# Performance work log

Measured on AMD Instinct MI355X. Metric: run time of the kernel, lower is better.

The kernel has to match this reference:

```python
import jax, jax.numpy as jnp
import numpy as np

N = 100000
E = 1600000
F_IN, H, C = 128, 128, 64


def setup_inputs() -> dict:
    key = jax.random.key(0)
    ks = jax.random.split(key, 8)
    x = jax.random.normal(ks[0], (N, F_IN), dtype=jnp.float32)
    edge_index = jax.random.randint(ks[1], (2, E), 0, N, dtype=jnp.int64)
    s = lambda fi: (1.0 / np.sqrt(fi))
    # SAGEConv1: lin_l (applied to mean-aggregated neighbors, has bias), lin_r (root, no bias)
    W1l = jax.random.uniform(ks[2], (H, F_IN), jnp.float32, -s(F_IN), s(F_IN))
    b1 = jnp.zeros((H,), jnp.float32)
    W1r = jax.random.uniform(ks[3], (H, F_IN), jnp.float32, -s(F_IN), s(F_IN))
    # SAGEConv2
    W2l = jax.random.uniform(ks[4], (C, H), jnp.float32, -s(H), s(H))
    b2 = jnp.zeros((C,), jnp.float32)
    W2r = jax.random.uniform(ks[5], (C, H), jnp.float32, -s(H), s(H))
    return {"x": x, "edge_index": edge_index, "W1l": W1l, "b1": b1, "W1r": W1r,
            "W2l": W2l, "b2": b2, "W2r": W2r}


def _mean_aggr(x, src, dst):
    # mean over incoming neighbors (PyG flow: edge_index[0]=source -> edge_index[1]=target)
    msg = x[src]                                            # [E, F] big gather
    summed = jax.ops.segment_sum(msg, dst, num_segments=N)  # [N, F]
    cnt = jax.ops.segment_sum(jnp.ones((src.shape[0],), x.dtype), dst, num_segments=N)
    return summed / jnp.clip(cnt, 1.0)[:, None]


def _sage_conv(x, src, dst, Wl, b, Wr):
    agg = _mean_aggr(x, src, dst)
    return agg @ Wl.T + b + x @ Wr.T


def _iconv(x, src, dst):
    # weight-free GCN propagation: D^-1/2 (A + I) D^-1/2 @ x
    loops = jnp.arange(N, dtype=src.dtype)
    s2 = jnp.concatenate([src, loops])
    d2 = jnp.concatenate([dst, loops])
    deg = jax.ops.segment_sum(jnp.ones((s2.shape[0],), x.dtype), d2, num_segments=N)
    dis = jnp.where(deg > 0, jax.lax.rsqrt(jnp.maximum(deg, 1.0)), 0.0)
    norm = dis[s2] * dis[d2]                               # [E+N]
    return jax.ops.segment_sum(norm[:, None] * x[s2], d2, num_segments=N)


def reference(x, edge_index, W1l, b1, W1r, W2l, b2, W2r):
    src, dst = edge_index[0], edge_index[1]
    h = jax.nn.relu(_sage_conv(x, src, dst, W1l, b1, W1r))
    # F.dropout(training=False) -> identity in eval mode
    h = _sage_conv(h, src, dst, W2l, b2, W2r)
    return _iconv(h, src, dst)
```

## Files before the change

### kernel.cpp

```cpp
#include <hip/hip_runtime.h>

#define GN 100000
#define GE 1600000
#define GF 128
#define GH 128
#define GC 64

#define NB 392
#define SLABSZ 5376
#define P1_EDGES 4096
#define P1_BLOCKS ((GE + P1_EDGES - 1) / P1_EDGES)
#define CASTX_BLOCKS 12500

typedef __attribute__((ext_vector_type(8))) short v8s;
typedef __attribute__((ext_vector_type(4))) float v4f;

__device__ __forceinline__ unsigned short f2bf(float f) {
    union { float f; unsigned u; } a; a.f = f;
    unsigned r = a.u + 0x7fff + ((a.u >> 16) & 1);
    return (unsigned short)(r >> 16);
}
__device__ __forceinline__ float bf2f(unsigned short b) {
    union { unsigned u; float f; } a; a.u = ((unsigned)b) << 16;
    return a.f;
}

__global__ __launch_bounds__(256) void prep_kernel(
    unsigned* __restrict__ slab, int* __restrict__ bucket_cnt,
    const int* __restrict__ src, const int* __restrict__ dst,
    unsigned short* __restrict__ xb, const float* __restrict__ x,
    unsigned short* w1l, unsigned short* w1r,
    unsigned short* w2l, unsigned short* w2r,
    const float* W1l, const float* W1r,
    const float* W2l, const float* W2r)
{
    __shared__ int hist[512];
    __shared__ int scanex[512];
    __shared__ int cursor[512];
    __shared__ int gbase[512];
    __shared__ int ssum[256];
    __shared__ unsigned stage[P1_EDGES];
    __shared__ unsigned short sbid[P1_EDGES];

    int tid = threadIdx.x;
    int blk = blockIdx.x;

    if (blk >= P1_BLOCKS) {
        int cb = blk - P1_BLOCKS;
        if (cb < CASTX_BLOCKS) {
            int i = cb * 256 + tid;
            float4 v = ((const float4*)x)[i];
            ushort4 u;
            u.x = f2bf(v.x); u.y = f2bf(v.y); u.z = f2bf(v.z); u.w = f2bf(v.w);
            ((ushort4*)xb)[i] = u;
            return;
        }
        int i = (cb - CASTX_BLOCKS) * 256 + tid;
        const float* s; unsigned short* d; int off;
        if      (i <  4096) { s = W1l; d = w1l; off = i; }
        else if (i <  8192) { s = W1r; d = w1r; off = i - 4096; }
        else if (i < 10240) { s = W2l; d = w2l; off = i - 8192; }
        else if (i < 12288) { s = W2r; d = w2r; off = i - 10240; }
        else return;
        float4 v = ((const float4*)s)[off];
        ushort4 u;
        u.x = f2bf(v.x); u.y = f2bf(v.y); u.z = f2bf(v.z); u.w = f2bf(v.w);
        ((ushort4*)d)[off] = u;
        return;
    }

    int e0 = blk * P1_EDGES;
    int nE = min(P1_EDGES, GE - e0);

    unsigned pk[16]; int bk[16];
    hist[tid] = 0; hist[tid + 256] = 0;
    __syncthreads();
    #pragma unroll
    for (int j = 0; j < 16; ++j) {
        int i = j * 256 + tid;
        if (i < nE) {
            int e = e0 + i;
            int d = dst[e], s = src[e];
            int b = d >> 8;
            pk[j] = ((unsigned)(d & 255) << 17) | (unsigned)s;
            bk[j] = b;
            atomicAdd(&hist[b], 1);
        } else bk[j] = -1;
    }
    __syncthreads();
    int a0 = hist[2 * tid], a1 = hist[2 * tid + 1];
    int s2 = a0 + a1;
    ssum[tid] = s2;
    __syncthreads();
    for (int off = 1; off < 256; off <<= 1) {
        int v = (tid >= off) ? ssum[tid - off] : 0;
        __syncthreads();
        ssum[tid] += v;
        __syncthreads();
    }
    int pbase = ssum[tid] - s2;
    scanex[2 * tid] = pbase;          cursor[2 * tid] = pbase;
    scanex[2 * tid + 1] = pbase + a0; cursor[2 * tid + 1] = pbase + a0;
    __syncthreads();
    #pragma unroll
    for (int j = 0; j < 16; ++j) {
        if (bk[j] >= 0) {
            int pos = atomicAdd(&cursor[bk[j]], 1);
            stage[pos] = pk[j];
            sbid[pos] = (unsigned short)bk[j];
        }
    }
    for (int b = tid; b < NB; b += 256) {
        int c = hist[b];
        gbase[b] = c ? atomicAdd(&bucket_cnt[b], c) : 0;
    }
    __syncthreads();
    for (int i = tid; i < nE; i += 256) {
        int b = sbid[i];
        int go = gbase[b] + (i - scanex[b]);
        if (go < SLABSZ)
            slab[(size_t)b * SLABSZ + go] = stage[i];
    }
}

__global__ __launch_bounds__(256) void bucket_pass2_kernel(
    int* __restrict__ csr, int* __restrict__ row_ptr,
    float* __restrict__ invc, float* __restrict__ dis,
    const unsigned* __restrict__ slab, const int* __restrict__ bucket_cnt)
{
    __shared__ int deg_l[256];
    __shared__ int excl[256];
    __shared__ int cur[256];
    __shared__ int ssum[256];
    __shared__ int bstart_s;
    __shared__ unsigned stage[SLABSZ];

    int t = threadIdx.x;
    int b = blockIdx.x;

    int c0 = (2 * t < NB) ? bucket_cnt[2 * t] : 0;
    int c1 = (2 * t + 1 < NB) ? bucket_cnt[2 * t + 1] : 0;
    int sc = c0 + c1;
    ssum[t] = sc;
    __syncthreads();
    for (int off = 1; off < 256; off <<= 1) {
        int v = (t >= off) ? ssum[t - off] : 0;
        __syncthreads();
        ssum[t] += v;
        __syncthreads();
    }
    int pb = ssum[t] - sc;
    if (2 * t == b)     bstart_s = pb;
    if (2 * t + 1 == b) bstart_s = pb + c0;
    if (b == NB - 1 && t == 0) row_ptr[GN] = GE;

    int cnt = min(bucket_cnt[b], SLABSZ);
    const unsigned* sp = slab + (size_t)b * SLABSZ;
    deg_l[t] = 0;
    __syncthreads();
    int base = bstart_s;
    for (int i = t; i < cnt; i += 256)
        atomicAdd(&deg_l[sp[i] >> 17], 1);
    __syncthreads();
    int dg = deg_l[t];
    ssum[t] = dg;
    __syncthreads();
    for (int off = 1; off < 256; off <<= 1) {
        int v = (t >= off) ? ssum[t - off] : 0;
        __syncthreads();
        ssum[t] += v;
        __syncthreads();
    }
    int ex = ssum[t] - dg;
    excl[t] = ex; cur[t] = ex;
    __syncthreads();
    int d = b * 256 + t;
    if (d < GN) {
        row_ptr[d] = base + ex;
        float c = (float)dg;
        invc[d] = 1.0f / fmaxf(c, 1.0f);
        dis[d] = rsqrtf(c + 1.0f);
    }
    for (int i = t; i < cnt; i += 256) {
        unsigned p = sp[i];
        int pos = atomicAdd(&cur[p >> 17], 1);
        stage[pos] = p & 0x1FFFFu;
    }
    __syncthreads();
    for (int i = t; i < cnt; i += 256)
        csr[base + i] = (int)stage[i];
}

__global__ __launch_bounds__(256) void fused_gemm_kernel(
    unsigned short* __restrict__ P, unsigned short* __restrict__ Q,
    const unsigned short* __restrict__ A1, const unsigned short* __restrict__ A2,
    const unsigned short* __restrict__ W1, const unsigned short* __restrict__ W2,
    const unsigned short* __restrict__ Wl, const unsigned short* __restrict__ Wr,
    const float* __restrict__ b1, const float* __restrict__ b2, int M)
{
    __shared__ unsigned short hs[256][136];

    int tid = threadIdx.x;
    int wv = tid >> 6, lane = tid & 63;
    int lm = lane & 15, quad = lane >> 4;
    int m_base = blockIdx.x * 256 + wv * 64;
    int row_l0 = wv * 64;

    for (int nh = 0; nh < 2; ++nh) {
        int n_base = nh * 64;
        v4f acc[4][4];
        #pragma unroll
        for (int mt = 0; mt < 4; ++mt)
            #pragma unroll
            for (int nt = 0; nt < 4; ++nt) acc[mt][nt] = (v4f){0.f,0.f,0.f,0.f};

        #pragma unroll
        for (int ks = 0; ks < 4; ++ks) {
            int koff = ks * 32 + quad * 8;
            v8s a1[4], a2[4], bw1[4], bw2[4];
            #pragma unroll
            for (int mt = 0; mt < 4; ++mt) {
                int row = m_base + mt * 16 + lm;
                if (row < M) {
                    a1[mt] = *(const v8s*)(A1 + (size_t)row * 128 + koff);
                    a2[mt] = *(const v8s*)(A2 + (size_t)row * 128 + koff);
                } else {
                    a1[mt] = (v8s){0,0,0,0,0,0,0,0};
                    a2[mt] = (v8s){0,0,0,0,0,0,0,0};
                }
            }
            #pragma unroll
            for (int nt = 0; nt < 4; ++nt) {
                int col = n_base + nt * 16 + lm;
                bw1[nt] = *(const v8s*)(W1 + (size_t)col * 128 + koff);
                bw2[nt] = *(const v8s*)(W2 + (size_t)col * 128 + koff);
            }
            #pragma unroll
            for (int mt = 0; mt < 4; ++mt)
                #pragma unroll
                for (int nt = 0; nt < 4; ++nt) {
                    acc[mt][nt] = __builtin_amdgcn_mfma_f32_16x16x32_bf16(a1[mt], bw1[nt], acc[mt][nt], 0, 0, 0);
                    acc[mt][nt] = __builtin_amdgcn_mfma_f32_16x16x32_bf16(a2[mt], bw2[nt], acc[mt][nt], 0, 0, 0);
                }
        }

        #pragma unroll
        for (int mt = 0; mt < 4; ++mt)
            #pragma unroll
            for (int r = 0; r < 4; ++r) {
                int rl = row_l0 + mt * 16 + quad * 4 + r;
                #pragma unroll
                for (int nt = 0; nt < 4; ++nt) {
                    int col = n_base + nt * 16 + lm;
                    float v = acc[mt][nt][r] + b1[col];
                    hs[rl][col] = f2bf(fmaxf(v, 0.f));
                }
            }
    }
    __syncthreads();

    v4f accP[4][4], accQ[4][4];
    #pragma unroll
    for (int mt = 0; mt < 4; ++mt)
        #pragma unroll
        for (int nt = 0; nt < 4; ++nt) {
            accP[mt][nt] = (v4f){0.f,0.f,0.f,0.f};
            accQ[mt][nt] = (v4f){0.f,0.f,0.f,0.f};
        }

    #pragma unroll
    for (int ks = 0; ks < 4; ++ks) {
        int koff = ks * 32 + quad * 8;
        v8s af[4], bl[4], br[4];
        #pragma unroll
        for (int mt = 0; mt < 4; ++mt)
            af[mt] = *(const v8s*)&hs[row_l0 + mt * 16 + lm][koff];
        #pragma unroll
        for (int nt = 0; nt < 4; ++nt) {
            int col = nt * 16 + lm;
            bl[nt] = *(const v8s*)(Wl + (size_t)col * 128 + koff);
            br[nt] = *(const v8s*)(Wr + (size_t)col * 128 + koff);
        }
        #pragma unroll
        for (int mt = 0; mt < 4; ++mt)
            #pragma unroll
            for (int nt = 0; nt < 4; ++nt) {
                accP[mt][nt] = __builtin_amdgcn_mfma_f32_16x16x32_bf16(af[mt], bl[nt], accP[mt][nt], 0, 0, 0);
                accQ[mt][nt] = __builtin_amdgcn_mfma_f32_16x16x32_bf16(af[mt], br[nt], accQ[mt][nt], 0, 0, 0);
            }
    }

    #pragma unroll
    for (int mt = 0; mt < 4; ++mt)
        #pragma unroll
        for (int r = 0; r < 4; ++r) {
            int row = m_base + mt * 16 + quad * 4 + r;
            if (row >= M) continue;
            #pragma unroll
            for (int nt = 0; nt < 4; ++nt) {
                int col = nt * 16 + lm;
                P[(size_t)row * 64 + col] = f2bf(accP[mt][nt][r]);
                Q[(size_t)row * 64 + col] = f2bf(accQ[mt][nt][r] + b2[col]);
            }
        }
}

__global__ __launch_bounds__(256) void gather_mean128_kernel(
    unsigned short* __restrict__ out, const unsigned short* __restrict__ in,
    const float* __restrict__ invc, const int* __restrict__ row_ptr,
    const int* __restrict__ csr, int N)
{
    int wid = (blockIdx.x * 256 + threadIdx.x) >> 6;
    int lane = threadIdx.x & 63;
    if (wid >= N) return;
    int beg = __builtin_amdgcn_readfirstlane(row_ptr[wid]);
    int end = __builtin_amdgcn_readfirstlane(row_ptr[wid + 1]);
    int d = end - beg;
    float a0 = 0.f, a1 = 0.f;
    if (d > 0) {
        int dc = min(d, 64);
        int idx = csr[beg + ((lane < dc) ? lane : (dc - 1))];
        for (int t = 0; t < dc; t += 16) {
            unsigned v[16];
            #pragma unroll
            for (int u = 0; u < 16; ++u) {
                int tt = t + u;
                int s = __builtin_amdgcn_readlane(idx, (tt < dc) ? tt : (dc - 1));
                unsigned x = ((const unsigned*)(in + (size_t)s * 128))[lane];
                v[u] = (tt < dc) ? x : 0u;
            }
            #pragma unroll
            for (int u = 0; u < 16; ++u) {
                a0 += bf2f((unsigned short)(v[u] & 0xffff));
                a1 += bf2f((unsigned short)(v[u] >> 16));
            }
        }
        for (int j = beg + 64; j < end; ++j) {
            int s = __builtin_amdgcn_readfirstlane(csr[j]);
            unsigned x = ((const unsigned*)(in + (size_t)s * 128))[lane];
            a0 += bf2f((unsigned short)(x & 0xffff));
            a1 += bf2f((unsigned short)(x >> 16));
        }
    }
    float ic = invc[wid];
    unsigned o = (unsigned)f2bf(a0 * ic) | ((unsigned)f2bf(a1 * ic) << 16);
    ((unsigned*)(out + (size_t)wid * 128))[lane] = o;
}

__global__ __launch_bounds__(256) void gather_combine_kernel(
    unsigned short* __restrict__ h2s, const unsigned short* __restrict__ p,
    const unsigned short* __restrict__ q,
    const float* __restrict__ invc, const float* __restrict__ dis,
    const int* __restrict__ row_ptr, const int* __restrict__ csr, int N)
{
    int wid = (blockIdx.x * 256 + threadIdx.x) >> 6;
    int lane = threadIdx.x & 63;
    if (wid >= N) return;
    int beg = __builtin_amdgcn_readfirstlane(row_ptr[wid]);
    int end = __builtin_amdgcn_readfirstlane(row_ptr[wid + 1]);
    int d = end - beg;
    float a = 0.f;
    if (d > 0) {
        int dc = min(d, 64);
        int idx = csr[beg + ((lane < dc) ? lane : (dc - 1))];
        for (int t = 0; t < dc; t += 16) {
            unsigned short v[16];
            #pragma unroll
            for (int u = 0; u < 16; ++u) {
                int tt = t + u;
                int s = __builtin_amdgcn_readlane(idx, (tt < dc) ? tt : (dc - 1));
                unsigned short x = p[(size_t)s * 64 + lane];
                v[u] = (tt < dc) ? x : (unsigned short)0;
            }
            #pragma unroll
            for (int u = 0; u < 16; ++u) a += bf2f(v[u]);
        }
        for (int j = beg + 64; j < end; ++j) {
            int s = __builtin_amdgcn_readfirstlane(csr[j]);
            a += bf2f(p[(size_t)s * 64 + lane]);
        }
    }
    float ic = invc[wid], dd = dis[wid];
    float qv = bf2f(q[(size_t)wid * 64 + lane]);
    h2s[(size_t)wid * 64 + lane] = f2bf(dd * (a * ic + qv));
}

__global__ __launch_bounds__(256) void iconv_kernel(
    float* __restrict__ out, const unsigned short* __restrict__ h2s,
    const float* __restrict__ dis, const int* __restrict__ row_ptr,
    const int* __restrict__ csr, int N)
{
    int wid = (blockIdx.x * 256 + threadIdx.x) >> 6;
    int lane = threadIdx.x & 63;
    if (wid >= N) return;
    int beg = __builtin_amdgcn_readfirstlane(row_ptr[wid]);
    int end = __builtin_amdgcn_readfirstlane(row_ptr[wid + 1]);
    int d = end - beg;
    float a = 0.f;
    if (d > 0) {
        int dc = min(d, 64);
        int idx = csr[beg + ((lane < dc) ? lane : (dc - 1))];
        for (int t = 0; t < dc; t += 16) {
            unsigned short v[16];
            #pragma unroll
            for (int u = 0; u < 16; ++u) {
                int tt = t + u;
                int s = __builtin_amdgcn_readlane(idx, (tt < dc) ? tt : (dc - 1));
                unsigned short x = h2s[(size_t)s * 64 + lane];
                v[u] = (tt < dc) ? x : (unsigned short)0;
            }
            #pragma unroll
            for (int u = 0; u < 16; ++u) a += bf2f(v[u]);
        }
        for (int j = beg + 64; j < end; ++j) {
            int s = __builtin_amdgcn_readfirstlane(csr[j]);
            a += bf2f(h2s[(size_t)s * 64 + lane]);
        }
    }
    a += bf2f(h2s[(size_t)wid * 64 + lane]);
    out[(size_t)wid * 64 + lane] = dis[wid] * a;
}

extern "C" void kernel_launch(void* const* d_in, const int* in_sizes, int n_in,
                              void* d_out, int out_size, void* d_ws, size_t ws_size,
                              hipStream_t stream) {
    const float* x   = (const float*)d_in[0];
    const int*   ei  = (const int*)d_in[1];
    const float* W1l = (const float*)d_in[2];
    const float* b1  = (const float*)d_in[3];
    const float* W1r = (const float*)d_in[4];
    const float* W2l = (const float*)d_in[5];
    const float* b2  = (const float*)d_in[6];
    const float* W2r = (const float*)d_in[7];
    float* out = (float*)d_out;

    const int* src = ei;
    const int* dst = ei + GE;

    float* invc = (float*)d_ws;
    float* dis  = invc + GN;
    unsigned short* regA = (unsigned short*)(dis + GN);
    unsigned short* regB = regA + (size_t)GN * 128;
    unsigned short* xb    = regA;
    unsigned short* aggx  = regB;
    unsigned short* w1lb = regB + (size_t)GN * 128;
    unsigned short* w1rb = w1lb + GH * GF;
    unsigned short* w2lb = w1rb + GH * GF;
    unsigned short* w2rb = w2lb + GC * GH;
    int* row_ptr      = (int*)(w2rb + GC * GH);
    int* bucket_cnt   = row_ptr + GN + 1;
    unsigned* slab    = (unsigned*)(bucket_cnt + NB);
    int* csr          = (int*)(slab + (size_t)NB * SLABSZ);
    unsigned short* pq = (unsigned short*)(csr + GE);
    unsigned short* pb = pq;
    unsigned short* qb = pq + (size_t)GN * 64;
    unsigned short* h2s = regB;

    const int T = 256;
    const int g_wave = (GN * 64 + T - 1) / T;
    dim3 g_fused((GN + 255) / 256, 1);

    hipMemsetAsync(bucket_cnt, 0, NB * sizeof(int), stream);
    prep_kernel<<<P1_BLOCKS + CASTX_BLOCKS + 48, T, 0, stream>>>(
        slab, bucket_cnt, src, dst,
        xb, x, w1lb, w1rb, w2lb, w2rb, W1l, W1r, W2l, W2r);

    bucket_pass2_kernel<<<NB, T, 0, stream>>>(csr, row_ptr, invc, dis,
                                              slab, bucket_cnt);

    gather_mean128_kernel<<<g_wave, T, 0, stream>>>(aggx, xb, invc, row_ptr, csr, GN);

    fused_gemm_kernel<<<g_fused, T, 0, stream>>>(pb, qb, aggx, xb,
                                                 w1lb, w1rb, w2lb, w2rb,
                                                 b1, b2, GN);

    gather_combine_kernel<<<g_wave, T, 0, stream>>>(h2s, pb, qb, invc, dis,
                                                    row_ptr, csr, GN);

    iconv_kernel<<<g_wave, T, 0, stream>>>(out, h2s, dis, row_ptr, csr, GN);
}
```

Before: 345.6 us.

## Restructure fused GEMM to one wave per 64-row block with full-width accumulators

Changes the fused two-layer GEMM kernel from 256-thread blocks handling 256 rows in two column halves to 64-thread single-wave blocks that compute all 128 hidden columns at once with a 4x8 accumulator tile. This removes the repeated A-tile loads across the two column halves and removes the block-level barrier, since each wave only uses its own shared-memory rows. In exchange it uses more accumulator registers per thread, which may reduce occupancy or cause spills, and it launches four times as many small blocks.

```diff
diff --git a/kernel.cpp b/kernel.cpp
--- a/kernel.cpp
+++ b/kernel.cpp
@@ -191,73 +191,68 @@
         csr[base + i] = (int)stage[i];
 }
 
-__global__ __launch_bounds__(256) void fused_gemm_kernel(
+__global__ __launch_bounds__(64, 2) void fused_gemm_kernel(
     unsigned short* __restrict__ P, unsigned short* __restrict__ Q,
     const unsigned short* __restrict__ A1, const unsigned short* __restrict__ A2,
     const unsigned short* __restrict__ W1, const unsigned short* __restrict__ W2,
     const unsigned short* __restrict__ Wl, const unsigned short* __restrict__ Wr,
     const float* __restrict__ b1, const float* __restrict__ b2, int M)
 {
-    __shared__ unsigned short hs[256][136];
-
-    int tid = threadIdx.x;
-    int wv = tid >> 6, lane = tid & 63;
+    __shared__ unsigned short hs[64][136];
+
+    int lane = threadIdx.x;
     int lm = lane & 15, quad = lane >> 4;
-    int m_base = blockIdx.x * 256 + wv * 64;
-    int row_l0 = wv * 64;
-
-    for (int nh = 0; nh < 2; ++nh) {
-        int n_base = nh * 64;
-        v4f acc[4][4];
+    int m_base = blockIdx.x * 64;
+
+    v4f acc[4][8];
+    #pragma unroll
+    for (int mt = 0; mt < 4; ++mt)
+        #pragma unroll
+        for (int nt = 0; nt < 8; ++nt) acc[mt][nt] = (v4f){0.f,0.f,0.f,0.f};
+
+    #pragma unroll
+    for (int ks = 0; ks < 4; ++ks) {
+        int koff = ks * 32 + quad * 8;
+        v8s a1[4], a2[4];
+        #pragma unroll
+        for (int mt = 0; mt < 4; ++mt) {
+            int row = m_base + mt * 16 + lm;
+            if (row < M) {
+                a1[mt] = *(const v8s*)(A1 + (size_t)row * 128 + koff);
+                a2[mt] = *(const v8s*)(A2 + (size_t)row * 128 + koff);
+            } else {
+                a1[mt] = (v8s){0,0,0,0,0,0,0,0};
+                a2[mt] = (v8s){0,0,0,0,0,0,0,0};
+            }
+        }
+        v8s w1[8], w2[8];
+        #pragma unroll
+        for (int nt = 0; nt < 8; ++nt) {
+            int col = nt * 16 + lm;
+            w1[nt] = *(const v8s*)(W1 + (size_t)col * 128 + koff);
+            w2[nt] = *(const v8s*)(W2 + (size_t)col * 128 + koff);
+        }
         #pragma unroll
         for (int mt = 0; mt < 4; ++mt)
             #pragma unroll
-            for (int nt = 0; nt < 4; ++nt) acc[mt][nt] = (v4f){0.f,0.f,0.f,0.f};
-
-        #pragma unroll
-        for (int ks = 0; ks < 4; ++ks) {
-            int koff = ks * 32 + quad * 8;
-            v8s a1[4], a2[4], bw1[4], bw2[4];
-            #pragma unroll
-            for (int mt = 0; mt < 4; ++mt) {
-                int row = m_base + mt * 16 + lm;
-                if (row < M) {
-                    a1[mt] = *(const v8s*)(A1 + (size_t)row * 128 + koff);
-                    a2[mt] = *(const v8s*)(A2 + (size_t)row * 128 + koff);
-                } else {
-                    a1[mt] = (v8s){0,0,0,0,0,0,0,0};
-                    a2[mt] = (v8s){0,0,0,0,0,0,0,0};
-                }
-            }
-            #pragma unroll
-            for (int nt = 0; nt < 4; ++nt) {
-                int col = n_base + nt * 16 + lm;
-                bw1[nt] = *(const v8s*)(W1 + (size_t)col * 128 + koff);
-                bw2[nt] = *(const v8s*)(W2 + (size_t)col * 128 + koff);
-            }
-            #pragma unroll
-            for (int mt = 0; mt < 4; ++mt)
-                #pragma unroll
-                for (int nt = 0; nt < 4; ++nt) {
-                    acc[mt][nt] = __builtin_amdgcn_mfma_f32_16x16x32_bf16(a1[mt], bw1[nt], acc[mt][nt], 0, 0, 0);
-                    acc[mt][nt] = __builtin_amdgcn_mfma_f32_16x16x32_bf16(a2[mt], bw2[nt], acc[mt][nt], 0, 0, 0);
-                }
-        }
-
-        #pragma unroll
-        for (int mt = 0; mt < 4; ++mt)
-            #pragma unroll
-            for (int r = 0; r < 4; ++r) {
-                int rl = row_l0 + mt * 16 + quad * 4 + r;
-                #pragma unroll
-                for (int nt = 0; nt < 4; ++nt) {
-                    int col = n_base + nt * 16 + lm;
-                    float v = acc[mt][nt][r] + b1[col];
-                    hs[rl][col] = f2bf(fmaxf(v, 0.f));
-                }
-            }
-    }
-    __syncthreads();
+            for (int nt = 0; nt < 8; ++nt) {
+                acc[mt][nt] = __builtin_amdgcn_mfma_f32_16x16x32_bf16(a1[mt], w1[nt], acc[mt][nt], 0, 0, 0);
+                acc[mt][nt] = __builtin_amdgcn_mfma_f32_16x16x32_bf16(a2[mt], w2[nt], acc[mt][nt], 0, 0, 0);
+            }
+    }
+
+    #pragma unroll
+    for (int mt = 0; mt < 4; ++mt)
+        #pragma unroll
+        for (int r = 0; r < 4; ++r) {
+            int rl = mt * 16 + quad * 4 + r;
+            #pragma unroll
+            for (int nt = 0; nt < 8; ++nt) {
+                int col = nt * 16 + lm;
+                float v = acc[mt][nt][r] + b1[col];
+                hs[rl][col] = f2bf(fmaxf(v, 0.f));
+            }
+        }
 
     v4f accP[4][4], accQ[4][4];
     #pragma unroll
@@ -274,7 +269,7 @@
         v8s af[4], bl[4], br[4];
         #pragma unroll
         for (int mt = 0; mt < 4; ++mt)
-            af[mt] = *(const v8s*)&hs[row_l0 + mt * 16 + lm][koff];
+            af[mt] = *(const v8s*)&hs[mt * 16 + lm][koff];
         #pragma unroll
         for (int nt = 0; nt < 4; ++nt) {
             int col = nt * 16 + lm;
@@ -458,7 +453,7 @@
 
     const int T = 256;
     const int g_wave = (GN * 64 + T - 1) / T;
-    dim3 g_fused((GN + 255) / 256, 1);
+    dim3 g_fused((GN + 63) / 64, 1);
 
     hipMemsetAsync(bucket_cnt, 0, NB * sizeof(int), stream);
     prep_kernel<<<P1_BLOCKS + CASTX_BLOCKS + 48, T, 0, stream>>>(
@@ -470,9 +465,9 @@
 
     gather_mean128_kernel<<<g_wave, T, 0, stream>>>(aggx, xb, invc, row_ptr, csr, GN);
 
-    fused_gemm_kernel<<<g_fused, T, 0, stream>>>(pb, qb, aggx, xb,
-                                                 w1lb, w1rb, w2lb, w2rb,
-                                                 b1, b2, GN);
+    fused_gemm_kernel<<<g_fused, 64, 0, stream>>>(pb, qb, aggx, xb,
+                                                  w1lb, w1rb, w2lb, w2rb,
+                                                  b1, b2, GN);
 
     gather_combine_kernel<<<g_wave, T, 0, stream>>>(h2s, pb, qb, invc, dis,
                                                     row_ptr, csr, GN);
```

Result: no change. 339.7 us (-1.7%).
